# Kernel tuning notes

Measured on AMD Instinct MI355X. Metric: run time of the kernel, lower is better.

Reference implementation:

```python
import jax, jax.numpy as jnp
import numpy as np

BS = 64
MUX_IN = 8192
MUX_OUT = 128
EPS = 1e-20
TEMP = 5.0  # temperature_update_tf(tempIncr, epoch=0, n_epochs) at step=0 -> constant tempIncr


def setup_inputs() -> dict:
    key = jax.random.key(0)
    k1, k2, k3 = jax.random.split(key, 3)
    logits = jax.random.normal(k1, (1, MUX_IN), dtype=jnp.float32)
    inpData = jax.random.normal(k2, (BS, MUX_IN), dtype=jnp.float32)
    u = jax.random.uniform(k3, (BS, 1, MUX_IN), dtype=jnp.float32)  # uniform noise -> Gumbel
    return {"logits": logits, "inpData": inpData, "u": u}


def reference(logits, inpData, u):
    # Gumbel noise, exactly as tf: -log(-log(U + 1e-20) + 1e-20)
    gn = -jnp.log(-jnp.log(u + EPS) + EPS)            # (BS, 1, M)
    perturbed = logits + gn                            # (1,M)+(BS,1,M) -> (BS,1,M)
    _, topk = jax.lax.top_k(perturbed, MUX_OUT)        # (BS, 1, K)
    topk = topk[:, 0, :]                               # squeeze axis=1 -> (BS, K)
    hard = jax.nn.one_hot(topk, MUX_IN, dtype=logits.dtype)   # (BS, K, M)
    # exclusive cumsum over the mux_out axis (axis=-2)
    cum_mask = jnp.cumsum(hard, axis=-2) - hard        # (BS, K, M)
    # log(exp(logits) * (1 - cumMask + eps)) == logits + log(1 - cumMask + eps)
    soft_logits = (logits + jnp.log(1.0 - cum_mask + EPS) + gn) / TEMP  # (BS, K, M)
    soft = jax.nn.softmax(soft_logits, axis=-1)
    # straight-through estimator
    return jax.lax.stop_gradient(hard - soft) + soft
```

## Files before the change

### kernel.cpp

```cpp
#include <hip/hip_runtime.h>
#include <math.h>

#define BS 64
#define MUX_IN 8192
#define MUX_OUT 128
#define EPSF 1e-20f

#define NFILL_BLOCKS 1984
#define NBLOCKS (64 + NFILL_BLOCKS)
#define OUT_FLOAT4 ((size_t)BS * MUX_OUT * MUX_IN / 4)

typedef unsigned int u32;
typedef unsigned long long u64;

__device__ __forceinline__ u32 sortable_f32(float f) {
    u32 b = __float_as_uint(f);
    return (b & 0x80000000u) ? ~b : (b | 0x80000000u);
}

__global__ __launch_bounds__(256) void fused_kernel(
        const float* __restrict__ logits,
        const float* __restrict__ u,
        int* __restrict__ topk,
        float* __restrict__ out) {
    const int t = threadIdx.x;

    if (blockIdx.x >= 64) {
        const size_t tid = (size_t)(blockIdx.x - 64) * 256 + t;
        const size_t nthreads = (size_t)NFILL_BLOCKS * 256;
        float4* __restrict__ o4 = (float4*)out;
        const float4 z = make_float4(0.f, 0.f, 0.f, 0.f);
        for (size_t p = tid; p < OUT_FLOAT4; p += nthreads) o4[p] = z;
        return;
    }

    const int b = blockIdx.x;
    const float* __restrict__ urow = u + (size_t)b * MUX_IN;

    u32 kv[32];
#pragma unroll
    for (int q = 0; q < 8; ++q) {
        const int base = q * 1024 + t * 4;
        const float4 uu = *(const float4*)(urow + base);
        const float4 lg = *(const float4*)(logits + base);
        float in0 = -logf(uu.x + EPSF) + EPSF; kv[q * 4 + 0] = sortable_f32(lg.x - logf(in0));
        float in1 = -logf(uu.y + EPSF) + EPSF; kv[q * 4 + 1] = sortable_f32(lg.y - logf(in1));
        float in2 = -logf(uu.z + EPSF) + EPSF; kv[q * 4 + 2] = sortable_f32(lg.z - logf(in2));
        float in3 = -logf(uu.w + EPSF) + EPSF; kv[q * 4 + 3] = sortable_f32(lg.w - logf(in3));
    }

    __shared__ u32 hist[4][256];
    __shared__ u32 suf[256];
    __shared__ int sK;
    __shared__ u32 sSel;
    __shared__ int cnt;
    __shared__ u64 list[256];

    if (t == 0) { sK = MUX_OUT; sSel = 0u; cnt = 0; }
    const int wv = t >> 6;

    for (int pass = 0; pass < 4; ++pass) {
        const int sh = 24 - pass * 8;
#pragma unroll
        for (int w = 0; w < 4; ++w) hist[w][t] = 0u;
        __syncthreads();

        const u32 mask = (pass == 0) ? 0u : (0xFFFFFFFFu << (sh + 8));
        const u32 sel = sSel;
        const int K = sK;
#pragma unroll
        for (int k = 0; k < 32; ++k) {
            if (((kv[k] ^ sel) & mask) == 0u)
                atomicAdd(&hist[wv][(kv[k] >> sh) & 255u], 1u);
        }
        __syncthreads();

        const u32 c = hist[0][t] + hist[1][t] + hist[2][t] + hist[3][t];
        suf[t] = c;
        __syncthreads();
        for (int off = 1; off < 256; off <<= 1) {
            const u32 v = suf[t] + ((t + off < 256) ? suf[t + off] : 0u);
            __syncthreads();
            suf[t] = v;
            __syncthreads();
        }
        const u32 gt = (t < 255) ? suf[t + 1] : 0u;
        if ((int)gt < K && (int)(gt + c) >= K) {
            sSel = sel | ((u32)t << sh);
            sK = K - (int)gt;
        }
        __syncthreads();
    }

    const u32 T = sSel;
#pragma unroll
    for (int k = 0; k < 32; ++k) {
        if (kv[k] >= T) {
            const int slot = atomicAdd(&cnt, 1);
            if (slot < 256) {
                const int gi = (k >> 2) * 1024 + t * 4 + (k & 3);
                list[slot] = ((u64)kv[k] << 32) | (u32)(MUX_IN - 1 - gi);
            }
        }
    }
    __syncthreads();
    int c0 = cnt; if (c0 > 256) c0 = 256;
    for (int idx = c0 + t; idx < 256; idx += 256) list[idx] = 0ull;
    __syncthreads();

    for (int kk = 2; kk <= 256; kk <<= 1) {
        for (int j = kk >> 1; j > 0; j >>= 1) {
            const int ixj = t ^ j;
            if (ixj > t) {
                const u64 a = list[t];
                const u64 bb = list[ixj];
                const bool desc = ((t & kk) == 0);
                if (desc ? (a < bb) : (a > bb)) { list[t] = bb; list[ixj] = a; }
            }
            __syncthreads();
        }
    }

    if (t < MUX_OUT) {
        const u64 e = list[t];
        topk[b * MUX_OUT + t] = MUX_IN - 1 - (int)(e & 0xFFFFFFFFull);
    }
}

__global__ __launch_bounds__(256) void ones_kernel(
        const int* __restrict__ topk,
        float* __restrict__ out) {
    const int r = blockIdx.x * 256 + threadIdx.x;
    out[(size_t)r * MUX_IN + topk[r]] = 1.0f;
}

extern "C" void kernel_launch(void* const* d_in, const int* in_sizes, int n_in,
                              void* d_out, int out_size, void* d_ws, size_t ws_size,
                              hipStream_t stream) {
    const float* logits = (const float*)d_in[0];
    const float* u = (const float*)d_in[2];
    float* out = (float*)d_out;
    int* topk = (int*)d_ws;

    fused_kernel<<<NBLOCKS, 256, 0, stream>>>(logits, u, topk, out);
    ones_kernel<<<(BS * MUX_OUT) / 256, 256, 0, stream>>>(topk, out);
}
```

Before: 42.45 us.

## Merge top-k and one-hot scatter into single cooperative kernel with grid barrier

Replaces the two-kernel sequence (fused top-k plus zero-fill, then a separate ones-scatter kernel) with one cooperative kernel of 512 blocks. Each block zero-fills its own 16 output rows, then waits on a global atomic counter that the 64 top-k blocks increment when they finish, and afterwards writes the 1.0 entries for its rows. This removes a kernel launch and the dependency gap between the kernels. In exchange it adds a memset launch for the counter, a spin-wait grid barrier, and a reliance on cooperative co-residency of all blocks. Fill parallelism also drops from 2048 to 512 blocks.

```diff
diff --git a/kernel.cpp b/kernel.cpp
--- a/kernel.cpp
+++ b/kernel.cpp
@@ -6,9 +6,9 @@
 #define MUX_OUT 128
 #define EPSF 1e-20f
 
-#define NFILL_BLOCKS 1984
-#define NBLOCKS (64 + NFILL_BLOCKS)
-#define OUT_FLOAT4 ((size_t)BS * MUX_OUT * MUX_IN / 4)
+#define NBLK 512
+#define ROWS_PER_BLK 16
+#define ROW4 (MUX_IN / 4)
 
 typedef unsigned int u32;
 typedef unsigned long long u64;
@@ -18,36 +18,14 @@
     return (b & 0x80000000u) ? ~b : (b | 0x80000000u);
 }
 
-__global__ __launch_bounds__(256) void fused_kernel(
+__global__ __launch_bounds__(256) void fused_all(
         const float* __restrict__ logits,
         const float* __restrict__ u,
         int* __restrict__ topk,
+        u32* __restrict__ done,
         float* __restrict__ out) {
     const int t = threadIdx.x;
-
-    if (blockIdx.x >= 64) {
-        const size_t tid = (size_t)(blockIdx.x - 64) * 256 + t;
-        const size_t nthreads = (size_t)NFILL_BLOCKS * 256;
-        float4* __restrict__ o4 = (float4*)out;
-        const float4 z = make_float4(0.f, 0.f, 0.f, 0.f);
-        for (size_t p = tid; p < OUT_FLOAT4; p += nthreads) o4[p] = z;
-        return;
-    }
-
-    const int b = blockIdx.x;
-    const float* __restrict__ urow = u + (size_t)b * MUX_IN;
-
-    u32 kv[32];
-#pragma unroll
-    for (int q = 0; q < 8; ++q) {
-        const int base = q * 1024 + t * 4;
-        const float4 uu = *(const float4*)(urow + base);
-        const float4 lg = *(const float4*)(logits + base);
-        float in0 = -logf(uu.x + EPSF) + EPSF; kv[q * 4 + 0] = sortable_f32(lg.x - logf(in0));
-        float in1 = -logf(uu.y + EPSF) + EPSF; kv[q * 4 + 1] = sortable_f32(lg.y - logf(in1));
-        float in2 = -logf(uu.z + EPSF) + EPSF; kv[q * 4 + 2] = sortable_f32(lg.z - logf(in2));
-        float in3 = -logf(uu.w + EPSF) + EPSF; kv[q * 4 + 3] = sortable_f32(lg.w - logf(in3));
-    }
+    const int blk = blockIdx.x;
 
     __shared__ u32 hist[4][256];
     __shared__ u32 suf[256];
@@ -56,82 +34,122 @@
     __shared__ int cnt;
     __shared__ u64 list[256];
 
-    if (t == 0) { sK = MUX_OUT; sSel = 0u; cnt = 0; }
-    const int wv = t >> 6;
+    if (blk < BS) {
+        const int b = blk;
+        const float* __restrict__ urow = u + (size_t)b * MUX_IN;
 
-    for (int pass = 0; pass < 4; ++pass) {
-        const int sh = 24 - pass * 8;
+        u32 kv[32];
 #pragma unroll
-        for (int w = 0; w < 4; ++w) hist[w][t] = 0u;
+        for (int q = 0; q < 8; ++q) {
+            const int base = q * 1024 + t * 4;
+            const float4 uu = *(const float4*)(urow + base);
+            const float4 lg = *(const float4*)(logits + base);
+            float in0 = -logf(uu.x + EPSF) + EPSF; kv[q * 4 + 0] = sortable_f32(lg.x - logf(in0));
+            float in1 = -logf(uu.y + EPSF) + EPSF; kv[q * 4 + 1] = sortable_f32(lg.y - logf(in1));
+            float in2 = -logf(uu.z + EPSF) + EPSF; kv[q * 4 + 2] = sortable_f32(lg.z - logf(in2));
+            float in3 = -logf(uu.w + EPSF) + EPSF; kv[q * 4 + 3] = sortable_f32(lg.w - logf(in3));
+        }
+
+        if (t == 0) { sK = MUX_OUT; sSel = 0u; cnt = 0; }
+        const int wv = t >> 6;
+
+        for (int pass = 0; pass < 4; ++pass) {
+            const int sh = 24 - pass * 8;
+#pragma unroll
+            for (int w = 0; w < 4; ++w) hist[w][t] = 0u;
+            __syncthreads();
+
+            const u32 mask = (pass == 0) ? 0u : (0xFFFFFFFFu << (sh + 8));
+            const u32 sel = sSel;
+            const int K = sK;
+#pragma unroll
+            for (int k = 0; k < 32; ++k) {
+                if (((kv[k] ^ sel) & mask) == 0u)
+                    atomicAdd(&hist[wv][(kv[k] >> sh) & 255u], 1u);
+            }
+            __syncthreads();
+
+            const u32 c = hist[0][t] + hist[1][t] + hist[2][t] + hist[3][t];
+            suf[t] = c;
+            __syncthreads();
+            for (int off = 1; off < 256; off <<= 1) {
+                const u32 v = suf[t] + ((t + off < 256) ? suf[t + off] : 0u);
+                __syncthreads();
+                suf[t] = v;
+                __syncthreads();
+            }
+            const u32 gt = (t < 255) ? suf[t + 1] : 0u;
+            if ((int)gt < K && (int)(gt + c) >= K) {
+                sSel = sel | ((u32)t << sh);
+                sK = K - (int)gt;
+            }
+            __syncthreads();
+        }
+
+        const u32 T = sSel;
+#pragma unroll
+        for (int k = 0; k < 32; ++k) {
+            if (kv[k] >= T) {
+                const int slot = atomicAdd(&cnt, 1);
+                if (slot < 256) {
+                    const int gi = (k >> 2) * 1024 + t * 4 + (k & 3);
+                    list[slot] = ((u64)kv[k] << 32) | (u32)(MUX_IN - 1 - gi);
+                }
+            }
+        }
+        __syncthreads();
+        int c0 = cnt; if (c0 > 256) c0 = 256;
+        for (int idx = c0 + t; idx < 256; idx += 256) list[idx] = 0ull;
         __syncthreads();
 
-        const u32 mask = (pass == 0) ? 0u : (0xFFFFFFFFu << (sh + 8));
-        const u32 sel = sSel;
-        const int K = sK;
-#pragma unroll
-        for (int k = 0; k < 32; ++k) {
-            if (((kv[k] ^ sel) & mask) == 0u)
-                atomicAdd(&hist[wv][(kv[k] >> sh) & 255u], 1u);
+        for (int kk = 2; kk <= 256; kk <<= 1) {
+            for (int j = kk >> 1; j > 0; j >>= 1) {
+                const int ixj = t ^ j;
+                if (ixj > t) {
+                    const u64 a = list[t];
+                    const u64 bb = list[ixj];
+                    const bool desc = ((t & kk) == 0);
+                    if (desc ? (a < bb) : (a > bb)) { list[t] = bb; list[ixj] = a; }
+                }
+                __syncthreads();
+            }
+        }
+
+        if (t < MUX_OUT) {
+            const u64 e = list[t];
+            topk[b * MUX_OUT + t] = MUX_IN - 1 - (int)(e & 0xFFFFFFFFull);
         }
         __syncthreads();
-
-        const u32 c = hist[0][t] + hist[1][t] + hist[2][t] + hist[3][t];
-        suf[t] = c;
-        __syncthreads();
-        for (int off = 1; off < 256; off <<= 1) {
-            const u32 v = suf[t] + ((t + off < 256) ? suf[t + off] : 0u);
-            __syncthreads();
-            suf[t] = v;
-            __syncthreads();
+        if (t == 0) {
+            __threadfence();
+            __hip_atomic_fetch_add(done, 1u, __ATOMIC_RELEASE,
+                                   __HIP_MEMORY_SCOPE_AGENT);
         }
-        const u32 gt = (t < 255) ? suf[t + 1] : 0u;
-        if ((int)gt < K && (int)(gt + c) >= K) {
-            sSel = sel | ((u32)t << sh);
-            sK = K - (int)gt;
-        }
-        __syncthreads();
     }
 
-    const u32 T = sSel;
-#pragma unroll
-    for (int k = 0; k < 32; ++k) {
-        if (kv[k] >= T) {
-            const int slot = atomicAdd(&cnt, 1);
-            if (slot < 256) {
-                const int gi = (k >> 2) * 1024 + t * 4 + (k & 3);
-                list[slot] = ((u64)kv[k] << 32) | (u32)(MUX_IN - 1 - gi);
-            }
+    {
+        float4* __restrict__ o4 =
+            (float4*)(out + (size_t)blk * ROWS_PER_BLK * MUX_IN);
+        const float4 z = make_float4(0.f, 0.f, 0.f, 0.f);
+        const int n4 = ROWS_PER_BLK * ROW4;
+        for (int p = t; p < n4; p += 256) o4[p] = z;
+    }
+
+    __syncthreads();
+    if (t == 0) {
+        while (__hip_atomic_load(done, __ATOMIC_ACQUIRE,
+                                 __HIP_MEMORY_SCOPE_AGENT) < BS) {
+            __builtin_amdgcn_s_sleep(2);
         }
     }
     __syncthreads();
-    int c0 = cnt; if (c0 > 256) c0 = 256;
-    for (int idx = c0 + t; idx < 256; idx += 256) list[idx] = 0ull;
-    __syncthreads();
 
-    for (int kk = 2; kk <= 256; kk <<= 1) {
-        for (int j = kk >> 1; j > 0; j >>= 1) {
-            const int ixj = t ^ j;
-            if (ixj > t) {
-                const u64 a = list[t];
-                const u64 bb = list[ixj];
-                const bool desc = ((t & kk) == 0);
-                if (desc ? (a < bb) : (a > bb)) { list[t] = bb; list[ixj] = a; }
-            }
-            __syncthreads();
-        }
+    if (t < ROWS_PER_BLK) {
+        const int row = blk * ROWS_PER_BLK + t;
+        const int idx = __hip_atomic_load(&topk[row], __ATOMIC_ACQUIRE,
+                                          __HIP_MEMORY_SCOPE_AGENT);
+        out[(size_t)row * MUX_IN + idx] = 1.0f;
     }
-
-    if (t < MUX_OUT) {
-        const u64 e = list[t];
-        topk[b * MUX_OUT + t] = MUX_IN - 1 - (int)(e & 0xFFFFFFFFull);
-    }
-}
-
-__global__ __launch_bounds__(256) void ones_kernel(
-        const int* __restrict__ topk,
-        float* __restrict__ out) {
-    const int r = blockIdx.x * 256 + threadIdx.x;
-    out[(size_t)r * MUX_IN + topk[r]] = 1.0f;
 }
 
 extern "C" void kernel_launch(void* const* d_in, const int* in_sizes, int n_in,
@@ -140,8 +158,14 @@
     const float* logits = (const float*)d_in[0];
     const float* u = (const float*)d_in[2];
     float* out = (float*)d_out;
+
     int* topk = (int*)d_ws;
+    u32* done = (u32*)((char*)d_ws + BS * MUX_OUT * sizeof(int));
 
-    fused_kernel<<<NBLOCKS, 256, 0, stream>>>(logits, u, topk, out);
-    ones_kernel<<<(BS * MUX_OUT) / 256, 256, 0, stream>>>(topk, out);
+    hipMemsetAsync(done, 0, sizeof(u32), stream);
+
+    void* args[] = {(void*)&logits, (void*)&u, (void*)&topk,
+                    (void*)&done, (void*)&out};
+    hipLaunchCooperativeKernel((const void*)fused_all, dim3(NBLK), dim3(256),
+                               args, 0, stream);
 }
```

After: 84.83 us. +99.8%, slower.
